# Kernel tuning notes

Measured on AMD Instinct MI355X. Metric: run time of the kernel, lower is better.

The kernel has to match this reference:

```python
import jax, jax.numpy as jnp
import numpy as np


def setup_inputs() -> dict:
    key = jax.random.key(0)
    k1, k2 = jax.random.split(key)
    B, L = 16384, 4096
    v = jax.random.normal(k1, (B, L), dtype=jnp.float32)
    z = jax.random.normal(k2, (B, L), dtype=jnp.float32)
    return {"v": v, "z": z}


def reference(v, z):
    # Householder reflection: z_new = z - 2 * v (v . z) / ||v||^2
    # Algebraically identical to the original's bmm(v v^T, z) formulation,
    # but avoids materializing the [B, L, L] outer product.
    vz = jnp.sum(v * z, axis=1, keepdims=True)       # [B, 1]
    norm_sq = jnp.sum(v * v, axis=1, keepdims=True)  # [B, 1]
    return z - 2.0 * v * (vz / norm_sq)
```

## Files before the change

kernel.cpp:

```cpp
#include <hip/hip_runtime.h>
#include <hip/hip_bf16.h>


#define L 4096
#define BLOCK 256
#define VEC_PER_THREAD (L / (BLOCK * 4))

__global__ __launch_bounds__(BLOCK) void hh_kernel(
    const float* __restrict__ v,
    const float* __restrict__ z,
    float* __restrict__ out)
{
    const int b   = blockIdx.x;
    const int tid = threadIdx.x;
    const long long base = (long long)b * L;

    const float4* v4 = reinterpret_cast<const float4*>(v + base);
    const float4* z4 = reinterpret_cast<const float4*>(z + base);
    float4*       o4 = reinterpret_cast<float4*>(out + base);

    float4 vr[VEC_PER_THREAD];
    float4 zr[VEC_PER_THREAD];
    float dot = 0.0f;
    float nsq = 0.0f;

#pragma unroll
    for (int i = 0; i < VEC_PER_THREAD; ++i) {
        vr[i] = v4[tid + i * BLOCK];
        zr[i] = z4[tid + i * BLOCK];
        dot += vr[i].x * zr[i].x + vr[i].y * zr[i].y
             + vr[i].z * zr[i].z + vr[i].w * zr[i].w;
        nsq += vr[i].x * vr[i].x + vr[i].y * vr[i].y
             + vr[i].z * vr[i].z + vr[i].w * vr[i].w;
    }

#pragma unroll
    for (int off = 32; off > 0; off >>= 1) {
        dot += __shfl_down(dot, off, 64);
        nsq += __shfl_down(nsq, off, 64);
    }

    __shared__ float sdot[BLOCK / 64];
    __shared__ float snsq[BLOCK / 64];
    __shared__ float sscale;
    const int wave = tid >> 6;
    const int lane = tid & 63;
    if (lane == 0) {
        sdot[wave] = dot;
        snsq[wave] = nsq;
    }
    __syncthreads();
    if (tid == 0) {
        float d = 0.0f, n = 0.0f;
#pragma unroll
        for (int w = 0; w < BLOCK / 64; ++w) { d += sdot[w]; n += snsq[w]; }
        sscale = -2.0f * d / n;
    }
    __syncthreads();
    const float s = sscale;

#pragma unroll
    for (int i = 0; i < VEC_PER_THREAD; ++i) {
        float4 o;
        o.x = zr[i].x + s * vr[i].x;
        o.y = zr[i].y + s * vr[i].y;
        o.z = zr[i].z + s * vr[i].z;
        o.w = zr[i].w + s * vr[i].w;
        o4[tid + i * BLOCK] = o;
    }
}

extern "C" void kernel_launch(void* const* d_in, const int* in_sizes, int n_in,
                              void* d_out, int out_size, void* d_ws, size_t ws_size,
                              hipStream_t stream) {
    const float* v = (const float*)d_in[0];
    const float* z = (const float*)d_in[1];
    float* out = (float*)d_out;

    const int B = in_sizes[0] / L;
    hh_kernel<<<B, BLOCK, 0, stream>>>(v, z, out);
}
```

Baseline: 577.8 us.

## Map one wavefront per row and use nontemporal output stores

```diff
diff --git a/kernel.cpp b/kernel.cpp
--- a/kernel.cpp
+++ b/kernel.cpp
@@ -1,72 +1,58 @@
 #include <hip/hip_runtime.h>
-#include <hip/hip_bf16.h>
 
 
 #define L 4096
-#define BLOCK 256
-#define VEC_PER_THREAD (L / (BLOCK * 4))
+#define WAVES_PER_BLOCK 4
+#define BLOCK (WAVES_PER_BLOCK * 64)
+#define F4 (L / (64 * 4))
 
-__global__ __launch_bounds__(BLOCK) void hh_kernel(
+typedef float f32x4 __attribute__((ext_vector_type(4)));
+
+__global__ __launch_bounds__(BLOCK, 1) void hh_kernel(
     const float* __restrict__ v,
     const float* __restrict__ z,
     float* __restrict__ out)
 {
-    const int b   = blockIdx.x;
-    const int tid = threadIdx.x;
-    const long long base = (long long)b * L;
+    const int wave = threadIdx.x >> 6;
+    const int lane = threadIdx.x & 63;
+    const long long row  = (long long)blockIdx.x * WAVES_PER_BLOCK + wave;
+    const long long base = row * (long long)L;
 
-    const float4* v4 = reinterpret_cast<const float4*>(v + base);
-    const float4* z4 = reinterpret_cast<const float4*>(z + base);
-    float4*       o4 = reinterpret_cast<float4*>(out + base);
+    const f32x4* v4 = reinterpret_cast<const f32x4*>(v + base);
+    const f32x4* z4 = reinterpret_cast<const f32x4*>(z + base);
+    f32x4*       o4 = reinterpret_cast<f32x4*>(out + base);
 
-    float4 vr[VEC_PER_THREAD];
-    float4 zr[VEC_PER_THREAD];
-    float dot = 0.0f;
-    float nsq = 0.0f;
+    f32x4 vr[F4];
+    f32x4 zr[F4];
 
 #pragma unroll
-    for (int i = 0; i < VEC_PER_THREAD; ++i) {
-        vr[i] = v4[tid + i * BLOCK];
-        zr[i] = z4[tid + i * BLOCK];
-        dot += vr[i].x * zr[i].x + vr[i].y * zr[i].y
-             + vr[i].z * zr[i].z + vr[i].w * zr[i].w;
-        nsq += vr[i].x * vr[i].x + vr[i].y * vr[i].y
-             + vr[i].z * vr[i].z + vr[i].w * vr[i].w;
+    for (int i = 0; i < F4; ++i) {
+        vr[i] = v4[lane + i * 64];
+        zr[i] = z4[lane + i * 64];
     }
+
+    f32x4 dotv = {0.f, 0.f, 0.f, 0.f};
+    f32x4 nsqv = {0.f, 0.f, 0.f, 0.f};
+#pragma unroll
+    for (int i = 0; i < F4; ++i) {
+        dotv += vr[i] * zr[i];
+        nsqv += vr[i] * vr[i];
+    }
+    float dot = dotv.x + dotv.y + dotv.z + dotv.w;
+    float nsq = nsqv.x + nsqv.y + nsqv.z + nsqv.w;
 
 #pragma unroll
     for (int off = 32; off > 0; off >>= 1) {
-        dot += __shfl_down(dot, off, 64);
-        nsq += __shfl_down(nsq, off, 64);
+        dot += __shfl_xor(dot, off, 64);
+        nsq += __shfl_xor(nsq, off, 64);
     }
 
-    __shared__ float sdot[BLOCK / 64];
-    __shared__ float snsq[BLOCK / 64];
-    __shared__ float sscale;
-    const int wave = tid >> 6;
-    const int lane = tid & 63;
-    if (lane == 0) {
-        sdot[wave] = dot;
-        snsq[wave] = nsq;
-    }
-    __syncthreads();
-    if (tid == 0) {
-        float d = 0.0f, n = 0.0f;
-#pragma unroll
-        for (int w = 0; w < BLOCK / 64; ++w) { d += sdot[w]; n += snsq[w]; }
-        sscale = -2.0f * d / n;
-    }
-    __syncthreads();
-    const float s = sscale;
+    const float s = -2.0f * dot / nsq;
 
 #pragma unroll
-    for (int i = 0; i < VEC_PER_THREAD; ++i) {
-        float4 o;
-        o.x = zr[i].x + s * vr[i].x;
-        o.y = zr[i].y + s * vr[i].y;
-        o.z = zr[i].z + s * vr[i].z;
-        o.w = zr[i].w + s * vr[i].w;
-        o4[tid + i * BLOCK] = o;
+    for (int i = 0; i < F4; ++i) {
+        f32x4 o = zr[i] + s * vr[i];
+        __builtin_nontemporal_store(o, &o4[lane + i * 64]);
     }
 }
 
@@ -78,5 +64,5 @@
     float* out = (float*)d_out;
 
     const int B = in_sizes[0] / L;
-    hh_kernel<<<B, BLOCK, 0, stream>>>(v, z, out);
+    hh_kernel<<<B / WAVES_PER_BLOCK, BLOCK, 0, stream>>>(v, z, out);
 }
```

After: 577.9 us. Within noise of the previous version (+0.0%).
